# Performance work log

Measured on AMD Instinct MI355X. Metric: run time of the kernel, lower is better.

Reference implementation:

```python
import math
import jax, jax.numpy as jnp
import numpy as np

B, S, D, H = 2, 2048, 768, 12
DK = D // H

def setup_inputs() -> dict:
    key = jax.random.key(0)
    ks = jax.random.split(key, 8)
    scale = 1.0 / math.sqrt(D)
    return {
        "Q": jax.random.normal(ks[0], (B, S, D), dtype=jnp.float32),
        "K": jax.random.normal(ks[1], (B, S, D), dtype=jnp.float32),
        "V": jax.random.normal(ks[2], (B, S, D), dtype=jnp.float32),
        "mask": jax.random.randint(ks[3], (B, 1, S, S), 0, 2, dtype=jnp.int32),
        "W_Q": jax.random.normal(ks[4], (D, D), dtype=jnp.float32) * scale,
        "W_K": jax.random.normal(ks[5], (D, D), dtype=jnp.float32) * scale,
        "W_V": jax.random.normal(ks[6], (D, D), dtype=jnp.float32) * scale,
        "W_O": jax.random.normal(ks[7], (D, D), dtype=jnp.float32) * scale,
    }

def reference(Q, K, V, mask, W_Q, W_K, W_V, W_O):
    # torch Linear: y = x @ W.T (weight shape [out, in], no bias)
    q = (Q @ W_Q.T).reshape(B, S, H, DK).transpose(0, 2, 1, 3)  # [B,H,S,dk]
    k = (K @ W_K.T).reshape(B, S, H, DK).transpose(0, 2, 1, 3)
    v = (V @ W_V.T).reshape(B, S, H, DK).transpose(0, 2, 1, 3)
    scores = jnp.einsum('bhqd,bhkd->bhqk', q, k) / math.sqrt(DK)
    scores = jnp.where(mask == 0, -jnp.inf, scores)
    weights = jax.nn.softmax(scores, axis=-1)
    weights = jnp.nan_to_num(weights, nan=0.0)
    out = jnp.einsum('bhqk,bhkd->bhqd', weights, v)  # [B,H,S,dk]
    out = out.transpose(0, 2, 1, 3).reshape(B, S, D)
    return out @ W_O.T
```

## Files before the change

### kernel.cpp

```cpp
#include <hip/hip_runtime.h>
#include <hip/hip_bf16.h>
#include <stdint.h>

typedef __attribute__((ext_vector_type(8))) short bf16x8;
typedef __attribute__((ext_vector_type(4))) short bf16x4;
typedef __attribute__((ext_vector_type(4))) float f32x4;
typedef __attribute__((ext_vector_type(16))) float f32x16;
typedef __attribute__((ext_vector_type(4))) unsigned short u16x4;

__device__ __forceinline__ unsigned short f2bf(float x) {
  union { __hip_bfloat16 h; unsigned short s; } u;
  u.h = __float2bfloat16(x);
  return u.s;
}
__device__ __forceinline__ unsigned int cvtpk(float lo, float hi) {
  unsigned int r;
  asm("v_cvt_pk_bf16_f32 %0, %1, %2" : "=v"(r) : "v"(lo), "v"(hi));
  return r;
}

__global__ __launch_bounds__(256) void maskpack_kernel(const int* __restrict__ mask,
                                                       unsigned int* __restrict__ mp,
                                                       int total) {
  int i = blockIdx.x * blockDim.x + threadIdx.x;
  const int lane = threadIdx.x & 63;
  const int stride = gridDim.x * blockDim.x;
  for (; i < total; i += stride) {
    unsigned long long b = __ballot(mask[i] != 0);
    if (lane == 0)       mp[i >> 5] = (unsigned int)b;
    else if (lane == 32) mp[i >> 5] = (unsigned int)(b >> 32);
  }
}

__global__ __launch_bounds__(256) void proj_gemm(
    const float* __restrict__ Qi, const float* __restrict__ Ki, const float* __restrict__ Vi,
    const float* __restrict__ Wq, const float* __restrict__ Wk, const float* __restrict__ Wv,
    unsigned short* __restrict__ qo, unsigned short* __restrict__ ko, unsigned short* __restrict__ vo) {
  constexpr int LDT = 56;
  __shared__ unsigned short As[128][LDT];
  __shared__ unsigned short Bs[128][LDT];
  const int z = blockIdx.z;
  const float* A = (z == 0) ? Qi : (z == 1) ? Ki : Vi;
  const float* W = (z == 0) ? Wq : (z == 1) ? Wk : Wv;
  const int m0 = blockIdx.y * 128, n0 = blockIdx.x * 128;
  const int t = threadIdx.x, lane = t & 63, w = t >> 6;
  const int wr = w >> 1, wc = w & 1;
  const int fr = lane & 15, fg = (lane >> 4) * 8;
  const int srow = t >> 3, sseg = t & 7;
  f32x4 acc[4][4] = {};
  for (int kk = 0; kk < 768; kk += 32) {
    for (int pp = 0; pp < 4; ++pp) {
      int row = srow + pp * 32;
      float4 fa = *(const float4*)&A[(size_t)(m0 + row) * 768 + kk + sseg * 4];
      float4 fb = *(const float4*)&W[(size_t)(n0 + row) * 768 + kk + sseg * 4];
      bf16x4 pa = {(short)f2bf(fa.x), (short)f2bf(fa.y), (short)f2bf(fa.z), (short)f2bf(fa.w)};
      bf16x4 pb = {(short)f2bf(fb.x), (short)f2bf(fb.y), (short)f2bf(fb.z), (short)f2bf(fb.w)};
      *(bf16x4*)&As[row][sseg * 4] = pa;
      *(bf16x4*)&Bs[row][sseg * 4] = pb;
    }
    __syncthreads();
    bf16x8 af[4], bfr[4];
    for (int i = 0; i < 4; ++i) af[i]  = *(const bf16x8*)&As[wr * 64 + i * 16 + fr][fg];
    for (int i = 0; i < 4; ++i) bfr[i] = *(const bf16x8*)&Bs[wc * 64 + i * 16 + fr][fg];
    for (int i = 0; i < 4; ++i)
      for (int j = 0; j < 4; ++j)
        acc[i][j] = __builtin_amdgcn_mfma_f32_16x16x32_bf16(af[i], bfr[j], acc[i][j], 0, 0, 0);
    __syncthreads();
  }
  if (z == 2) {
    for (int i = 0; i < 4; ++i)
      for (int j = 0; j < 4; ++j) {
        int m = m0 + wr * 64 + i * 16 + (lane >> 4) * 4;
        int n = n0 + wc * 64 + j * 16 + fr;
        int b = m >> 11, s = m & 2047, hd = n >> 6, dk = n & 63;
        u16x4 pk;
        for (int r = 0; r < 4; ++r) pk[r] = f2bf(acc[i][j][r]);
        *(u16x4*)&vo[((size_t)(b * 12 + hd) * 64 + dk) * 2048 + s] = pk;
      }
  } else {
    unsigned short* O = (z == 0) ? qo : ko;
    const float scale = (z == 0) ? 0.18033688f : 1.0f;
    for (int i = 0; i < 4; ++i)
      for (int j = 0; j < 4; ++j)
        for (int r = 0; r < 4; ++r) {
          int m = m0 + wr * 64 + i * 16 + (lane >> 4) * 4 + r;
          int n = n0 + wc * 64 + j * 16 + fr;
          int b = m >> 11, s = m & 2047, hd = n >> 6, dk = n & 63;
          O[((size_t)(b * 12 + hd) * 2048 + s) * 64 + dk] = f2bf(acc[i][j][r] * scale);
        }
  }
}

__global__ __launch_bounds__(256) void out_gemm(
    const unsigned short* __restrict__ Ain, const float* __restrict__ W,
    float* __restrict__ Out) {
  constexpr int LDT = 56;
  __shared__ unsigned short As[128][LDT];
  __shared__ unsigned short Bs[128][LDT];
  const int m0 = blockIdx.y * 128, n0 = blockIdx.x * 128;
  const int t = threadIdx.x, lane = t & 63, w = t >> 6;
  const int wr = w >> 1, wc = w & 1;
  const int fr = lane & 15, fg = (lane >> 4) * 8;
  f32x4 acc[4][4] = {};
  for (int kk = 0; kk < 768; kk += 32) {
    {
      int row = t >> 2, seg = t & 3;
      for (int pp = 0; pp < 2; ++pp) {
        bf16x8 va = *(const bf16x8*)&Ain[(size_t)(m0 + row + pp * 64) * 768 + kk + seg * 8];
        *(bf16x8*)&As[row + pp * 64][seg * 8] = va;
      }
      int row2 = t >> 3, seg2 = t & 7;
      for (int pp = 0; pp < 4; ++pp) {
        float4 fb = *(const float4*)&W[(size_t)(n0 + row2 + pp * 32) * 768 + kk + seg2 * 4];
        bf16x4 pb = {(short)f2bf(fb.x), (short)f2bf(fb.y), (short)f2bf(fb.z), (short)f2bf(fb.w)};
        *(bf16x4*)&Bs[row2 + pp * 32][seg2 * 4] = pb;
      }
    }
    __syncthreads();
    bf16x8 af[4], bfr[4];
    for (int i = 0; i < 4; ++i) af[i]  = *(const bf16x8*)&As[wr * 64 + i * 16 + fr][fg];
    for (int i = 0; i < 4; ++i) bfr[i] = *(const bf16x8*)&Bs[wc * 64 + i * 16 + fr][fg];
    for (int i = 0; i < 4; ++i)
      for (int j = 0; j < 4; ++j)
        acc[i][j] = __builtin_amdgcn_mfma_f32_16x16x32_bf16(af[i], bfr[j], acc[i][j], 0, 0, 0);
    __syncthreads();
  }
  for (int i = 0; i < 4; ++i)
    for (int j = 0; j < 4; ++j)
      for (int r = 0; r < 4; ++r) {
        int m = m0 + wr * 64 + i * 16 + (lane >> 4) * 4 + r;
        int n = n0 + wc * 64 + j * 16 + fr;
        Out[(size_t)m * 768 + n] = acc[i][j][r];
      }
}

#define PVSTEP(P, OFF, A0, A1) { \
  unsigned int a0 = cvtpk(P[OFF + 0], P[OFF + 1]), a1 = cvtpk(P[OFF + 2], P[OFF + 3]); \
  unsigned int b0 = cvtpk(P[OFF + 4], P[OFF + 5]), b1 = cvtpk(P[OFF + 6], P[OFF + 7]); \
  int s0 = h ? (int)a0 : (int)b0, s1 = h ? (int)a1 : (int)b1; \
  unsigned int r0 = (unsigned int)__shfl_xor(s0, 32, 64); \
  unsigned int r1 = (unsigned int)__shfl_xor(s1, 32, 64); \
  union { unsigned int u[4]; bf16x8 v; } bfu; \
  bfu.u[0] = h ? r0 : a0; bfu.u[1] = h ? r1 : a1; \
  bfu.u[2] = h ? b0 : r0; bfu.u[3] = h ? b1 : r1; \
  acc0 = __builtin_amdgcn_mfma_f32_32x32x16_bf16(A0, bfu.v, acc0, 0, 0, 0); \
  acc1 = __builtin_amdgcn_mfma_f32_32x32x16_bf16(A1, bfu.v, acc1, 0, 0, 0); }

__global__ __launch_bounds__(128) void attn_kernel(
    const unsigned short* __restrict__ qh, const unsigned short* __restrict__ kh,
    const unsigned short* __restrict__ vh, const unsigned int* __restrict__ mp,
    unsigned short* __restrict__ ao) {
  __shared__ unsigned short Kl[2][64][64];
  __shared__ unsigned short Vl[2][64][64];
  const int t = threadIdx.x, lane = t & 63, w = t >> 6;
  const int bh = blockIdx.y, bb = bh / 12, hh = bh % 12;
  const int q0 = blockIdx.x * 64 + w * 32;
  const int qc = lane & 31, h = lane >> 5;
  const int q = q0 + qc;
  const unsigned short* qrow = qh + ((size_t)bh * 2048 + q) * 64;
  bf16x8 bq[4];
#pragma unroll
  for (int kc = 0; kc < 4; ++kc) bq[kc] = *(const bf16x8*)(qrow + kc * 16 + h * 8);
  const unsigned int* mrow = mp + ((size_t)bb * 2048 + q) * 64;
  const unsigned short* kgb = kh + (size_t)bh * 2048 * 64;
  const unsigned short* vgb = vh + (size_t)bh * 64 * 2048;
  f32x16 acc0 = {}, acc1 = {};
  float m_run = -1e30f, l_run = 0.f;
  bf16x8 stK[4], stV[4];
  auto LOADT = [&](int KT) {
#pragma unroll
    for (int i = 0; i < 4; ++i) {
      const int g = t + 128 * i, row = g >> 3, cc = g & 7;
      stK[i] = *(const bf16x8*)(kgb + (size_t)(KT + row) * 64 + cc * 8);
      stV[i] = *(const bf16x8*)(vgb + (size_t)row * 2048 + KT + cc * 8);
    }
  };
  auto STORET = [&](int BUF) {
#pragma unroll
    for (int i = 0; i < 4; ++i) {
      const int g = t + 128 * i, row = g >> 3, cc = (g & 7) ^ (row & 7);
      *(bf16x8*)&Kl[BUF][row][cc * 8] = stK[i];
      *(bf16x8*)&Vl[BUF][row][cc * 8] = stV[i];
    }
  };
  LOADT(0);
  STORET(0);
  __syncthreads();
#pragma unroll 2
  for (int it = 0; it < 32; ++it) {
    const int kt = it * 64, cur = it & 1;
    const bool more = it < 31;
    if (more) LOADT(kt + 64);
    unsigned long long msh = (*(const unsigned long long*)(mrow + (kt >> 5))) >> (4 * h);
    bf16x8 ka0[4], ka1[4];
#pragma unroll
    for (int kc = 0; kc < 4; ++kc) {
      ka0[kc] = *(const bf16x8*)&Kl[cur][qc][((kc * 2 + h) ^ (qc & 7)) * 8];
      ka1[kc] = *(const bf16x8*)&Kl[cur][32 + qc][((kc * 2 + h) ^ (qc & 7)) * 8];
    }
    f32x16 sc0 = {}, sc1 = {};
#pragma unroll
    for (int kc = 0; kc < 4; ++kc) {
      sc0 = __builtin_amdgcn_mfma_f32_32x32x16_bf16(ka0[kc], bq[kc], sc0, 0, 0, 0);
      sc1 = __builtin_amdgcn_mfma_f32_32x32x16_bf16(ka1[kc], bq[kc], sc1, 0, 0, 0);
    }
    bf16x8 va0[4], va1[4];
#pragma unroll
    for (int kf = 0; kf < 4; ++kf) {
      va0[kf] = *(const bf16x8*)&Vl[cur][qc][((kf * 2 + h) ^ (qc & 7)) * 8];
      va1[kf] = *(const bf16x8*)&Vl[cur][32 + qc][((kf * 2 + h) ^ (qc & 7)) * 8];
    }
    float tmax = -3.0e38f;
#pragma unroll
    for (int r = 0; r < 16; ++r) {
      const int sh = (r & 3) + 8 * (r >> 2);
      if (!((msh >> sh) & 1ULL))        sc0[r] = -3.0e38f;
      if (!((msh >> (32 + sh)) & 1ULL)) sc1[r] = -3.0e38f;
      tmax = fmaxf(tmax, fmaxf(sc0[r], sc1[r]));
    }
    tmax = fmaxf(tmax, __shfl_xor(tmax, 32, 64));
    const float mnew = fmaxf(m_run, tmax);
    const float scl = exp2f(m_run - mnew);
    m_run = mnew;
    float tsum = 0.f;
#pragma unroll
    for (int r = 0; r < 16; ++r) {
      float p0 = exp2f(sc0[r] - mnew);
      float p1 = exp2f(sc1[r] - mnew);
      sc0[r] = p0; sc1[r] = p1;
      tsum += p0 + p1;
    }
    tsum += __shfl_xor(tsum, 32, 64);
    l_run = l_run * scl + tsum;
#pragma unroll
    for (int e = 0; e < 16; ++e) { acc0[e] *= scl; acc1[e] *= scl; }
    PVSTEP(sc0, 0, va0[0], va1[0]);
    PVSTEP(sc0, 8, va0[1], va1[1]);
    PVSTEP(sc1, 0, va0[2], va1[2]);
    PVSTEP(sc1, 8, va0[3], va1[3]);
    if (more) STORET(1 - cur);
    __syncthreads();
  }
  const float inv = (l_run > 0.f) ? 1.0f / l_run : 0.f;
  unsigned short* orow = ao + ((size_t)bb * 2048 + q) * 768 + hh * 64;
#pragma unroll
  for (int rr = 0; rr < 4; ++rr) {
    u16x4 o0, o1;
#pragma unroll
    for (int j = 0; j < 4; ++j) {
      o0[j] = f2bf(acc0[rr * 4 + j] * inv);
      o1[j] = f2bf(acc1[rr * 4 + j] * inv);
    }
    const int d0 = 8 * rr + 4 * h;
    *(u16x4*)&orow[d0] = o0;
    *(u16x4*)&orow[32 + d0] = o1;
  }
}

extern "C" void kernel_launch(void* const* d_in, const int* in_sizes, int n_in,
                              void* d_out, int out_size, void* d_ws, size_t ws_size,
                              hipStream_t stream) {
  const float* Q  = (const float*)d_in[0];
  const float* K  = (const float*)d_in[1];
  const float* V  = (const float*)d_in[2];
  const int*   mask = (const int*)d_in[3];
  const float* WQ = (const float*)d_in[4];
  const float* WK = (const float*)d_in[5];
  const float* WV = (const float*)d_in[6];
  const float* WO = (const float*)d_in[7];
  float* out = (float*)d_out;

  char* ws = (char*)d_ws;
  unsigned short* qh = (unsigned short*)(ws + 0);
  unsigned short* kh = (unsigned short*)(ws + 6291456);
  unsigned short* vh = (unsigned short*)(ws + 12582912);
  unsigned short* ao = (unsigned short*)(ws + 18874368);
  unsigned int*   mp = (unsigned int*)(ws + 25165824);

  maskpack_kernel<<<dim3(2048), 256, 0, stream>>>(mask, mp, 2 * 2048 * 2048);
  proj_gemm<<<dim3(6, 32, 3), 256, 0, stream>>>(Q, K, V, WQ, WK, WV, qh, kh, vh);
  attn_kernel<<<dim3(32, 24), 128, 0, stream>>>(qh, kh, vh, mp, ao);
  out_gemm<<<dim3(6, 32), 256, 0, stream>>>(ao, WO, out);
}
```

Baseline: 175.6 us.

## Split attention KV range across waves with LDS merge, direct global loads

Restructures the attention kernel so each 256-thread block handles 32 queries and its four waves each process a quarter of the key range, reading K/V fragments straight from global memory instead of staging them in double-buffered LDS. The partial softmax states are merged through shared memory at the end. It also adds XCD-aware block remapping so heads stay local to one L2, a lazy rescale that only updates the running max when it grows by more than a threshold, permlane32 swaps in place of shuffles, and tree reductions. The aim is more parallelism and fewer syncs in the main loop, at the cost of uncoalesced global loads that rely on cache, plus extra LDS traffic for the merge.

```diff
diff --git a/kernel.cpp b/kernel.cpp
--- a/kernel.cpp
+++ b/kernel.cpp
@@ -134,27 +134,20 @@
       }
 }
 
-#define PVSTEP(P, OFF, A0, A1) { \
-  unsigned int a0 = cvtpk(P[OFF + 0], P[OFF + 1]), a1 = cvtpk(P[OFF + 2], P[OFF + 3]); \
-  unsigned int b0 = cvtpk(P[OFF + 4], P[OFF + 5]), b1 = cvtpk(P[OFF + 6], P[OFF + 7]); \
-  int s0 = h ? (int)a0 : (int)b0, s1 = h ? (int)a1 : (int)b1; \
-  unsigned int r0 = (unsigned int)__shfl_xor(s0, 32, 64); \
-  unsigned int r1 = (unsigned int)__shfl_xor(s1, 32, 64); \
-  union { unsigned int u[4]; bf16x8 v; } bfu; \
-  bfu.u[0] = h ? r0 : a0; bfu.u[1] = h ? r1 : a1; \
-  bfu.u[2] = h ? b0 : r0; bfu.u[3] = h ? b1 : r1; \
-  acc0 = __builtin_amdgcn_mfma_f32_32x32x16_bf16(A0, bfu.v, acc0, 0, 0, 0); \
-  acc1 = __builtin_amdgcn_mfma_f32_32x32x16_bf16(A1, bfu.v, acc1, 0, 0, 0); }
-
-__global__ __launch_bounds__(128) void attn_kernel(
+__global__ __launch_bounds__(256) void attn_kernel(
     const unsigned short* __restrict__ qh, const unsigned short* __restrict__ kh,
     const unsigned short* __restrict__ vh, const unsigned int* __restrict__ mp,
     unsigned short* __restrict__ ao) {
-  __shared__ unsigned short Kl[2][64][64];
-  __shared__ unsigned short Vl[2][64][64];
+  __shared__ float Sacc[4][32][64];
+  __shared__ float Sm[4][64];
+  __shared__ float Sl[4][64];
   const int t = threadIdx.x, lane = t & 63, w = t >> 6;
-  const int bh = blockIdx.y, bb = bh / 12, hh = bh % 12;
-  const int q0 = blockIdx.x * 64 + w * 32;
+  const int bid = blockIdx.x;
+  const int xcd = bid & 7, ixd = bid >> 3;
+  const int bh = xcd * 3 + (ixd >> 6);
+  const int qb = ixd & 63;
+  const int bb = bh / 12, hh = bh % 12;
+  const int q0 = qb * 32;
   const int qc = lane & 31, h = lane >> 5;
   const int q = q0 + qc;
   const unsigned short* qrow = qh + ((size_t)bh * 2048 + q) * 64;
@@ -166,37 +159,14 @@
   const unsigned short* vgb = vh + (size_t)bh * 64 * 2048;
   f32x16 acc0 = {}, acc1 = {};
   float m_run = -1e30f, l_run = 0.f;
-  bf16x8 stK[4], stV[4];
-  auto LOADT = [&](int KT) {
-#pragma unroll
-    for (int i = 0; i < 4; ++i) {
-      const int g = t + 128 * i, row = g >> 3, cc = g & 7;
-      stK[i] = *(const bf16x8*)(kgb + (size_t)(KT + row) * 64 + cc * 8);
-      stV[i] = *(const bf16x8*)(vgb + (size_t)row * 2048 + KT + cc * 8);
-    }
-  };
-  auto STORET = [&](int BUF) {
-#pragma unroll
-    for (int i = 0; i < 4; ++i) {
-      const int g = t + 128 * i, row = g >> 3, cc = (g & 7) ^ (row & 7);
-      *(bf16x8*)&Kl[BUF][row][cc * 8] = stK[i];
-      *(bf16x8*)&Vl[BUF][row][cc * 8] = stV[i];
-    }
-  };
-  LOADT(0);
-  STORET(0);
-  __syncthreads();
-#pragma unroll 2
-  for (int it = 0; it < 32; ++it) {
-    const int kt = it * 64, cur = it & 1;
-    const bool more = it < 31;
-    if (more) LOADT(kt + 64);
-    unsigned long long msh = (*(const unsigned long long*)(mrow + (kt >> 5))) >> (4 * h);
+
+  for (int it = 0; it < 8; ++it) {
+    const int kt = (w * 8 + it) * 64;
     bf16x8 ka0[4], ka1[4];
 #pragma unroll
     for (int kc = 0; kc < 4; ++kc) {
-      ka0[kc] = *(const bf16x8*)&Kl[cur][qc][((kc * 2 + h) ^ (qc & 7)) * 8];
-      ka1[kc] = *(const bf16x8*)&Kl[cur][32 + qc][((kc * 2 + h) ^ (qc & 7)) * 8];
+      ka0[kc] = *(const bf16x8*)(kgb + (size_t)(kt + qc) * 64 + (kc * 2 + h) * 8);
+      ka1[kc] = *(const bf16x8*)(kgb + (size_t)(kt + 32 + qc) * 64 + (kc * 2 + h) * 8);
     }
     f32x16 sc0 = {}, sc1 = {};
 #pragma unroll
@@ -207,53 +177,89 @@
     bf16x8 va0[4], va1[4];
 #pragma unroll
     for (int kf = 0; kf < 4; ++kf) {
-      va0[kf] = *(const bf16x8*)&Vl[cur][qc][((kf * 2 + h) ^ (qc & 7)) * 8];
-      va1[kf] = *(const bf16x8*)&Vl[cur][32 + qc][((kf * 2 + h) ^ (qc & 7)) * 8];
-    }
-    float tmax = -3.0e38f;
+      va0[kf] = *(const bf16x8*)(vgb + (size_t)qc * 2048 + kt + (kf * 2 + h) * 8);
+      va1[kf] = *(const bf16x8*)(vgb + (size_t)(32 + qc) * 2048 + kt + (kf * 2 + h) * 8);
+    }
+    unsigned long long mw = *(const unsigned long long*)(mrow + (kt >> 5));
+    unsigned int lo32 = (unsigned int)mw, hi32 = (unsigned int)(mw >> 32);
+    unsigned int wl = __builtin_amdgcn_alignbit(hi32, lo32, 4 * h);
+    unsigned int whd = hi32 >> (4 * h);
 #pragma unroll
     for (int r = 0; r < 16; ++r) {
       const int sh = (r & 3) + 8 * (r >> 2);
-      if (!((msh >> sh) & 1ULL))        sc0[r] = -3.0e38f;
-      if (!((msh >> (32 + sh)) & 1ULL)) sc1[r] = -3.0e38f;
-      tmax = fmaxf(tmax, fmaxf(sc0[r], sc1[r]));
-    }
-    tmax = fmaxf(tmax, __shfl_xor(tmax, 32, 64));
-    const float mnew = fmaxf(m_run, tmax);
-    const float scl = exp2f(m_run - mnew);
-    m_run = mnew;
-    float tsum = 0.f;
+      sc0[r] = ((wl >> sh) & 1u) ? sc0[r] : -3.0e38f;
+      sc1[r] = ((whd >> sh) & 1u) ? sc1[r] : -3.0e38f;
+    }
+    float mA[8];
+#pragma unroll
+    for (int i = 0; i < 8; ++i)
+      mA[i] = fmaxf(fmaxf(sc0[i], sc0[i + 8]), fmaxf(sc1[i], sc1[i + 8]));
+    float mB0 = fmaxf(mA[0], mA[4]), mB1 = fmaxf(mA[1], mA[5]);
+    float mB2 = fmaxf(mA[2], mA[6]), mB3 = fmaxf(mA[3], mA[7]);
+    float m1 = fmaxf(fmaxf(mB0, mB1), fmaxf(mB2, mB3));
+    float tmax = fmaxf(m1, __shfl_xor(m1, 32, 64));
+    if (__any(tmax > m_run + 8.0f)) {
+      float mnew = fmaxf(m_run, tmax);
+      float scl = exp2f(m_run - mnew);
+      m_run = mnew;
+      l_run *= scl;
+#pragma unroll
+      for (int e = 0; e < 16; ++e) { acc0[e] *= scl; acc1[e] *= scl; }
+    }
 #pragma unroll
     for (int r = 0; r < 16; ++r) {
-      float p0 = exp2f(sc0[r] - mnew);
-      float p1 = exp2f(sc1[r] - mnew);
-      sc0[r] = p0; sc1[r] = p1;
-      tsum += p0 + p1;
-    }
-    tsum += __shfl_xor(tsum, 32, 64);
-    l_run = l_run * scl + tsum;
-#pragma unroll
-    for (int e = 0; e < 16; ++e) { acc0[e] *= scl; acc1[e] *= scl; }
-    PVSTEP(sc0, 0, va0[0], va1[0]);
-    PVSTEP(sc0, 8, va0[1], va1[1]);
-    PVSTEP(sc1, 0, va0[2], va1[2]);
-    PVSTEP(sc1, 8, va0[3], va1[3]);
-    if (more) STORET(1 - cur);
-    __syncthreads();
-  }
-  const float inv = (l_run > 0.f) ? 1.0f / l_run : 0.f;
+      sc0[r] = exp2f(sc0[r] - m_run);
+      sc1[r] = exp2f(sc1[r] - m_run);
+    }
+    float sA[8];
+#pragma unroll
+    for (int i = 0; i < 8; ++i)
+      sA[i] = (sc0[i] + sc0[i + 8]) + (sc1[i] + sc1[i + 8]);
+    float sB0 = sA[0] + sA[4], sB1 = sA[1] + sA[5], sB2 = sA[2] + sA[6], sB3 = sA[3] + sA[7];
+    float s1 = (sB0 + sB1) + (sB2 + sB3);
+    l_run += s1 + __shfl_xor(s1, 32, 64);
+#define PVQ(P, OFF, A0, A1) { \
+    unsigned int a0 = cvtpk(P[OFF + 0], P[OFF + 1]), a1 = cvtpk(P[OFF + 2], P[OFF + 3]); \
+    unsigned int b0 = cvtpk(P[OFF + 4], P[OFF + 5]), b1 = cvtpk(P[OFF + 6], P[OFF + 7]); \
+    asm("v_permlane32_swap_b32 %0, %1" : "+v"(a0), "+v"(b0)); \
+    asm("v_permlane32_swap_b32 %0, %1" : "+v"(a1), "+v"(b1)); \
+    union { unsigned int u[4]; bf16x8 v; } bfu; \
+    bfu.u[0] = a0; bfu.u[1] = a1; bfu.u[2] = b0; bfu.u[3] = b1; \
+    acc0 = __builtin_amdgcn_mfma_f32_32x32x16_bf16(A0, bfu.v, acc0, 0, 0, 0); \
+    acc1 = __builtin_amdgcn_mfma_f32_32x32x16_bf16(A1, bfu.v, acc1, 0, 0, 0); }
+    PVQ(sc0, 0, va0[0], va1[0]);
+    PVQ(sc0, 8, va0[1], va1[1]);
+    PVQ(sc1, 0, va0[2], va1[2]);
+    PVQ(sc1, 8, va0[3], va1[3]);
+#undef PVQ
+  }
+  Sm[w][lane] = m_run;
+  Sl[w][lane] = l_run;
+#pragma unroll
+  for (int e = 0; e < 16; ++e) Sacc[w][e][lane] = acc0[e];
+#pragma unroll
+  for (int e = 0; e < 16; ++e) Sacc[w][16 + e][lane] = acc1[e];
+  __syncthreads();
+  float pm0 = Sm[0][lane], pm1 = Sm[1][lane], pm2 = Sm[2][lane], pm3 = Sm[3][lane];
+  float M = fmaxf(fmaxf(pm0, pm1), fmaxf(pm2, pm3));
+  float w0 = exp2f(pm0 - M), w1 = exp2f(pm1 - M), w2 = exp2f(pm2 - M), w3 = exp2f(pm3 - M);
+  float L = Sl[0][lane] * w0 + Sl[1][lane] * w1 + Sl[2][lane] * w2 + Sl[3][lane] * w3;
+  float inv = (L > 0.f) ? 1.0f / L : 0.f;
   unsigned short* orow = ao + ((size_t)bb * 2048 + q) * 768 + hh * 64;
 #pragma unroll
-  for (int rr = 0; rr < 4; ++rr) {
-    u16x4 o0, o1;
+  for (int g = 0; g < 2; ++g) {
+    const int e0 = w * 8 + g * 4;
+    const int base = (e0 >= 16) ? 32 : 0;
+    const int er0 = e0 & 15;
+    const int d0 = base + 8 * (er0 >> 2) + 4 * h;
+    u16x4 pk4;
 #pragma unroll
     for (int j = 0; j < 4; ++j) {
-      o0[j] = f2bf(acc0[rr * 4 + j] * inv);
-      o1[j] = f2bf(acc1[rr * 4 + j] * inv);
-    }
-    const int d0 = 8 * rr + 4 * h;
-    *(u16x4*)&orow[d0] = o0;
-    *(u16x4*)&orow[32 + d0] = o1;
+      float v = (Sacc[0][e0 + j][lane] * w0 + Sacc[1][e0 + j][lane] * w1 +
+                 Sacc[2][e0 + j][lane] * w2 + Sacc[3][e0 + j][lane] * w3) * inv;
+      pk4[j] = f2bf(v);
+    }
+    *(u16x4*)&orow[d0] = pk4;
   }
 }
 
@@ -279,6 +285,6 @@
 
   maskpack_kernel<<<dim3(2048), 256, 0, stream>>>(mask, mp, 2 * 2048 * 2048);
   proj_gemm<<<dim3(6, 32, 3), 256, 0, stream>>>(Q, K, V, WQ, WK, WV, qh, kh, vh);
-  attn_kernel<<<dim3(32, 24), 128, 0, stream>>>(qh, kh, vh, mp, ao);
+  attn_kernel<<<dim3(1536), 256, 0, stream>>>(qh, kh, vh, mp, ao);
   out_gemm<<<dim3(6, 32), 256, 0, stream>>>(ao, WO, out);
 }
```

Measured after the change: 189.5 us. +7.9%, slower.
